# Kernel tuning notes

Hardware: AMD Instinct MI355X
Metric: run time of the kernel (lower is better)

## Reference

```python
import jax, jax.numpy as jnp
import numpy as np

EPS = 1e-5

def _ln(x):
    # non-affine LayerNorm over last dim
    m = jnp.mean(x, axis=-1, keepdims=True)
    v = jnp.var(x, axis=-1, keepdims=True)
    return (x - m) / jnp.sqrt(v + EPS)

def setup_inputs() -> dict:
    key = jax.random.key(0)
    ks = jax.random.split(key, 6)
    B, D_in, H = 16384, 512, 512
    bound_i = 1.0 / np.sqrt(D_in)
    bound_h = 1.0 / np.sqrt(H)
    x = jax.random.normal(ks[0], (B, D_in), dtype=jnp.float32)
    hx = jax.random.normal(ks[1], (B, H), dtype=jnp.float32)
    W_i2h = jax.random.uniform(ks[2], (3 * H, D_in), minval=-bound_i, maxval=bound_i, dtype=jnp.float32)
    b_i2h = jax.random.uniform(ks[3], (3 * H,), minval=-bound_i, maxval=bound_i, dtype=jnp.float32)
    W_h2h = jax.random.uniform(ks[4], (3 * H, H), minval=-bound_h, maxval=bound_h, dtype=jnp.float32)
    b_h2h = jax.random.uniform(ks[5], (3 * H,), minval=-bound_h, maxval=bound_h, dtype=jnp.float32)
    return {"x": x, "hx": hx, "W_i2h": W_i2h, "b_i2h": b_i2h, "W_h2h": W_h2h, "b_h2h": b_h2h}

def reference(x, hx, W_i2h, b_i2h, W_h2h, b_h2h):
    H = hx.shape[-1]
    xt = x @ W_i2h.T + b_i2h        # [B, 3H]
    ht = hx @ W_h2h.T + b_h2h       # [B, 3H]
    x_new = xt[:, 2 * H:]
    h_new = ht[:, 2 * H:]
    gates = jax.nn.sigmoid(_ln(xt[:, : 2 * H]) + _ln(ht[:, : 2 * H]))
    r_t = gates[:, :H]
    z_t = gates[:, H:]
    n_t = jnp.tanh(_ln(x_new) + r_t * _ln(h_new))
    h_t = z_t * hx + (1.0 - z_t) * n_t
    return h_t
```

## Files before the change

### kernel.cpp

```cpp
#include <hip/hip_runtime.h>

#define M_ROWS 16384
#define N_COLS 1536
#define K_DIM  512
#define H_DIM  512

typedef __attribute__((ext_vector_type(8))) short short8;
typedef __attribute__((ext_vector_type(16))) float f32x16;

__device__ __forceinline__ unsigned short f2bf(float f) {
  unsigned u = __float_as_uint(f);
  u += 0x7fffu + ((u >> 16) & 1u);
  return (unsigned short)(u >> 16);
}
__device__ __forceinline__ float bf2f(unsigned short h) {
  return __uint_as_float(((unsigned)h) << 16);
}

__device__ __forceinline__ void gload_lds16(const void* g, void* l) {
  __builtin_amdgcn_global_load_lds((const __attribute__((address_space(1))) void*)g,
                                   (__attribute__((address_space(3))) void*)l,
                                   16, 0, 0);
}

__global__ __launch_bounds__(256) void cvt_all(
    const float* __restrict__ x, const float* __restrict__ hx,
    const float* __restrict__ Wi, const float* __restrict__ Wh,
    unsigned short* __restrict__ xb, unsigned short* __restrict__ hxb,
    unsigned short* __restrict__ Wib, unsigned short* __restrict__ Whb) {
  int i = blockIdx.x * blockDim.x + threadIdx.x;
  const float* s; unsigned short* d; int off;
  if (i < 2097152)      { s = x;  d = xb;  off = i; }
  else if (i < 4194304) { s = hx; d = hxb; off = i - 2097152; }
  else if (i < 4390912) { s = Wi; d = Wib; off = i - 4194304; }
  else                  { s = Wh; d = Whb; off = i - 4390912; }
  float4 f = ((const float4*)s)[off];
  ushort4 u;
  u.x = f2bf(f.x); u.y = f2bf(f.y); u.z = f2bf(f.z); u.w = f2bf(f.w);
  ((ushort4*)d)[off] = u;
}

__global__ __launch_bounds__(256, 4) void gemm_bf16(
    const unsigned short* __restrict__ xb, const unsigned short* __restrict__ hxb,
    const unsigned short* __restrict__ Wib, const unsigned short* __restrict__ Whb,
    const float* __restrict__ b_i2h, const float* __restrict__ b_h2h,
    unsigned short* __restrict__ xt, unsigned short* __restrict__ ht) {
  const int mat = blockIdx.z;
  const unsigned short* A  = mat ? hxb : xb;
  const unsigned short* Bw = mat ? Whb : Wib;
  const float* bias        = mat ? b_h2h : b_i2h;
  unsigned short* outp     = mat ? ht : xt;

  const int m0 = blockIdx.x * 128;
  const int n0 = blockIdx.y * 128;

  __shared__ short lds[2 * 128 * 64];
  short* ldsA = lds;
  short* ldsB = lds + 128 * 64;

  const int t = threadIdx.x;
  const int w = t >> 6, lane = t & 63;
  const int w_row = w >> 1, w_col = w & 1;
  const int l31 = lane & 31, h = lane >> 5;

  f32x16 acc[2][2];
#pragma unroll
  for (int i = 0; i < 2; ++i)
#pragma unroll
    for (int j = 0; j < 2; ++j)
#pragma unroll
      for (int r = 0; r < 16; ++r) acc[i][j][r] = 0.f;

  const int srow = lane >> 3;
  const int scol = ((lane & 7) ^ srow) * 8;

  for (int k0 = 0; k0 < K_DIM; k0 += 64) {
#pragma unroll
    for (int q = 0; q < 4; ++q) {
      const int base_row = w * 32 + q * 8;
      gload_lds16(A  + (size_t)(m0 + base_row + srow) * K_DIM + k0 + scol,
                  &ldsA[base_row * 64]);
      gload_lds16(Bw + (size_t)(n0 + base_row + srow) * K_DIM + k0 + scol,
                  &ldsB[base_row * 64]);
    }
    __syncthreads();
#pragma unroll
    for (int kk = 0; kk < 4; ++kk) {
      const int chunk = ((kk * 2 + h) ^ (l31 & 7)) * 8;
      short8 af[2], bf[2];
#pragma unroll
      for (int i = 0; i < 2; ++i)
        af[i] = *(const short8*)&ldsA[(w_row * 64 + i * 32 + l31) * 64 + chunk];
#pragma unroll
      for (int j = 0; j < 2; ++j)
        bf[j] = *(const short8*)&ldsB[(w_col * 64 + j * 32 + l31) * 64 + chunk];
#pragma unroll
      for (int i = 0; i < 2; ++i)
#pragma unroll
        for (int j = 0; j < 2; ++j)
          acc[i][j] = __builtin_amdgcn_mfma_f32_32x32x16_bf16(af[i], bf[j], acc[i][j], 0, 0, 0);
    }
    __syncthreads();
  }

  const float biasj0 = bias[n0 + w_col * 64 + l31];
  const float biasj1 = bias[n0 + w_col * 64 + 32 + l31];

#pragma unroll
  for (int i = 0; i < 2; ++i) {
#pragma unroll
    for (int g = 0; g < 4; ++g) {
#pragma unroll
      for (int d = 0; d < 4; ++d) {
        const int reg = g * 4 + d;
        const int row = d + 8 * g + 4 * h;
        ushort2 pk;
        pk.x = f2bf(acc[i][0][reg] + biasj0);
        pk.y = f2bf(acc[i][1][reg] + biasj1);
        *(ushort2*)(outp + (size_t)(m0 + w_row * 64 + i * 32 + row) * N_COLS +
                    n0 + w_col * 64 + 2 * l31) = pk;
      }
    }
  }
}

__global__ __launch_bounds__(256, 6) void finalize_kernel(
    const unsigned short* __restrict__ xt, const unsigned short* __restrict__ ht,
    const unsigned short* __restrict__ hxb, float* __restrict__ out) {
  const int w = threadIdx.x >> 6, lane = threadIdx.x & 63;
  const int b = blockIdx.x * 4 + w;
  const size_t rb = (size_t)b * N_COLS;

  const short8 sxr = *(const short8*)&xt[rb + 8 * lane];
  const short8 sxz = *(const short8*)&xt[rb + 512 + 8 * lane];
  const short8 sxn = *(const short8*)&xt[rb + 1024 + 8 * lane];
  const short8 shr = *(const short8*)&ht[rb + 8 * lane];
  const short8 shz = *(const short8*)&ht[rb + 512 + 8 * lane];
  const short8 shn = *(const short8*)&ht[rb + 1024 + 8 * lane];
  const int base4 = 64 * (lane >> 3) + 4 * (lane & 7);
  const unsigned short* hxrow = hxb + (size_t)b * H_DIM;
  const ushort4 hx0u = *(const ushort4*)&hxrow[base4];
  const ushort4 hx1u = *(const ushort4*)&hxrow[base4 + 32];

  float pr[8] = {0.f, 0.f, 0.f, 0.f, 0.f, 0.f, 0.f, 0.f};
#pragma unroll
  for (int k = 0; k < 8; ++k) {
    const float xr = bf2f((unsigned short)sxr[k]);
    const float xz = bf2f((unsigned short)sxz[k]);
    const float xn = bf2f((unsigned short)sxn[k]);
    const float hr = bf2f((unsigned short)shr[k]);
    const float hz = bf2f((unsigned short)shz[k]);
    const float hn = bf2f((unsigned short)shn[k]);
    pr[0] += xr + xz;
    pr[1] += xr * xr + xz * xz;
    pr[2] += xn;
    pr[3] += xn * xn;
    pr[4] += hr + hz;
    pr[5] += hr * hr + hz * hz;
    pr[6] += hn;
    pr[7] += hn * hn;
  }
#pragma unroll
  for (int msk = 1; msk < 64; msk <<= 1)
#pragma unroll
    for (int k = 0; k < 8; ++k) pr[k] += __shfl_xor(pr[k], msk);

  const float inv2H = 1.f / 1024.f, invH = 1.f / 512.f;
  const float mx0 = pr[0] * inv2H;
  const float ix0 = rsqrtf(pr[1] * inv2H - mx0 * mx0 + 1e-5f);
  const float mx1 = pr[2] * invH;
  const float ix1 = rsqrtf(pr[3] * invH - mx1 * mx1 + 1e-5f);
  const float mh0 = pr[4] * inv2H;
  const float ih0 = rsqrtf(pr[5] * inv2H - mh0 * mh0 + 1e-5f);
  const float mh1 = pr[6] * invH;
  const float ih1 = rsqrtf(pr[7] * invH - mh1 * mh1 + 1e-5f);

  auto calc = [&](float xrv, float xzv, float xnv, float hrv, float hzv,
                  float hnv, float hxs) -> float {
    float ar = (xrv - mx0) * ix0 + (hrv - mh0) * ih0;
    float az = (xzv - mx0) * ix0 + (hzv - mh0) * ih0;
    float r = 1.f / (1.f + __expf(-ar));
    float z = 1.f / (1.f + __expf(-az));
    float arg = (xnv - mx1) * ix1 + r * ((hnv - mh1) * ih1);
    float e2 = __expf(2.f * arg);
    float nn = (e2 - 1.f) / (e2 + 1.f);
    return z * hxs + (1.f - z) * nn;
  };

  float* orow = out + (size_t)b * H_DIM;

  float4 r0, r1;
  float* r0p = (float*)&r0;
  float* r1p = (float*)&r1;
  const unsigned short hx0a[4] = {hx0u.x, hx0u.y, hx0u.z, hx0u.w};
  const unsigned short hx1a[4] = {hx1u.x, hx1u.y, hx1u.z, hx1u.w};
#pragma unroll
  for (int k = 0; k < 4; ++k) {
    r0p[k] = calc(bf2f((unsigned short)sxr[2 * k]), bf2f((unsigned short)sxz[2 * k]),
                  bf2f((unsigned short)sxn[2 * k]), bf2f((unsigned short)shr[2 * k]),
                  bf2f((unsigned short)shz[2 * k]), bf2f((unsigned short)shn[2 * k]),
                  bf2f(hx0a[k]));
    r1p[k] = calc(bf2f((unsigned short)sxr[2 * k + 1]), bf2f((unsigned short)sxz[2 * k + 1]),
                  bf2f((unsigned short)sxn[2 * k + 1]), bf2f((unsigned short)shr[2 * k + 1]),
                  bf2f((unsigned short)shz[2 * k + 1]), bf2f((unsigned short)shn[2 * k + 1]),
                  bf2f(hx1a[k]));
  }
  *(float4*)&orow[base4] = r0;
  *(float4*)&orow[base4 + 32] = r1;
}

extern "C" void kernel_launch(void* const* d_in, const int* in_sizes, int n_in,
                              void* d_out, int out_size, void* d_ws, size_t ws_size,
                              hipStream_t stream) {
  const float* x  = (const float*)d_in[0];
  const float* hx = (const float*)d_in[1];
  const float* Wi = (const float*)d_in[2];
  const float* bi = (const float*)d_in[3];
  const float* Wh = (const float*)d_in[4];
  const float* bh = (const float*)d_in[5];
  float* out = (float*)d_out;

  char* ws = (char*)d_ws;
  unsigned short* xb  = (unsigned short*)(ws);
  unsigned short* hxb = (unsigned short*)(ws + 16777216);
  unsigned short* Wib = (unsigned short*)(ws + 33554432);
  unsigned short* Whb = (unsigned short*)(ws + 35127296);
  unsigned short* xt  = (unsigned short*)(ws + 36700160);
  unsigned short* ht  = (unsigned short*)(ws + 87031808);

  cvt_all<<<17920, 256, 0, stream>>>(x, hx, Wi, Wh, xb, hxb, Wib, Whb);

  gemm_bf16<<<dim3(M_ROWS / 128, N_COLS / 128, 2), 256, 0, stream>>>(
      xb, hxb, Wib, Whb, bi, bh, xt, ht);

  finalize_kernel<<<M_ROWS / 4, 256, 0, stream>>>(xt, ht, hxb, out);
}
```

Before: 206.4 us.

## Fuse GRU finalize into GEMM via per-row-block atomic completion counter

Each GEMM block now computes four N-tiles for one 128-row panel and one matrix, which reuses the A panel from cache across tiles. Blocks that share a row panel increment an atomic counter, and the last of the six runs the LayerNorm/GRU finalize for those 128 rows. This removes the separate finalize launch and lets finalize overlap with other blocks' GEMM work. The cost is a grid of only 768 blocks with serial tiles, which lowers parallelism, and the finalize tail runs on a single block per panel.

New measurement: 441.8 us. +114.0%, slower.

```diff
diff --git a/kernel.cpp b/kernel.cpp
--- a/kernel.cpp
+++ b/kernel.cpp
@@ -27,8 +27,10 @@
     const float* __restrict__ x, const float* __restrict__ hx,
     const float* __restrict__ Wi, const float* __restrict__ Wh,
     unsigned short* __restrict__ xb, unsigned short* __restrict__ hxb,
-    unsigned short* __restrict__ Wib, unsigned short* __restrict__ Whb) {
+    unsigned short* __restrict__ Wib, unsigned short* __restrict__ Whb,
+    int* __restrict__ cnt) {
   int i = blockIdx.x * blockDim.x + threadIdx.x;
+  if (blockIdx.x == 0 && threadIdx.x < 128) cnt[threadIdx.x] = 0;
   const float* s; unsigned short* d; int off;
   if (i < 2097152)      { s = x;  d = xb;  off = i; }
   else if (i < 4194304) { s = hx; d = hxb; off = i - 2097152; }
@@ -40,173 +42,185 @@
   ((ushort4*)d)[off] = u;
 }
 
-__global__ __launch_bounds__(256, 4) void gemm_bf16(
+__global__ __launch_bounds__(256, 4) void gemm_fin(
     const unsigned short* __restrict__ xb, const unsigned short* __restrict__ hxb,
     const unsigned short* __restrict__ Wib, const unsigned short* __restrict__ Whb,
     const float* __restrict__ b_i2h, const float* __restrict__ b_h2h,
-    unsigned short* __restrict__ xt, unsigned short* __restrict__ ht) {
-  const int mat = blockIdx.z;
+    unsigned short* __restrict__ xt, unsigned short* __restrict__ ht,
+    float* __restrict__ out, int* __restrict__ cnt) {
+  const int bid = blockIdx.x;
+  const int mp  = bid / 6;
+  const int rem = bid % 6;
+  const int mat = rem & 1;
+  const int ng  = rem >> 1;
+  const int m0  = mp * 128;
+
   const unsigned short* A  = mat ? hxb : xb;
   const unsigned short* Bw = mat ? Whb : Wib;
   const float* bias        = mat ? b_h2h : b_i2h;
   unsigned short* outp     = mat ? ht : xt;
 
-  const int m0 = blockIdx.x * 128;
-  const int n0 = blockIdx.y * 128;
-
   __shared__ short lds[2 * 128 * 64];
   short* ldsA = lds;
   short* ldsB = lds + 128 * 64;
+  __shared__ int dofin;
 
   const int t = threadIdx.x;
   const int w = t >> 6, lane = t & 63;
   const int w_row = w >> 1, w_col = w & 1;
   const int l31 = lane & 31, h = lane >> 5;
-
-  f32x16 acc[2][2];
-#pragma unroll
-  for (int i = 0; i < 2; ++i)
-#pragma unroll
-    for (int j = 0; j < 2; ++j)
-#pragma unroll
-      for (int r = 0; r < 16; ++r) acc[i][j][r] = 0.f;
-
   const int srow = lane >> 3;
   const int scol = ((lane & 7) ^ srow) * 8;
 
-  for (int k0 = 0; k0 < K_DIM; k0 += 64) {
-#pragma unroll
-    for (int q = 0; q < 4; ++q) {
-      const int base_row = w * 32 + q * 8;
-      gload_lds16(A  + (size_t)(m0 + base_row + srow) * K_DIM + k0 + scol,
-                  &ldsA[base_row * 64]);
-      gload_lds16(Bw + (size_t)(n0 + base_row + srow) * K_DIM + k0 + scol,
-                  &ldsB[base_row * 64]);
-    }
-    __syncthreads();
-#pragma unroll
-    for (int kk = 0; kk < 4; ++kk) {
-      const int chunk = ((kk * 2 + h) ^ (l31 & 7)) * 8;
-      short8 af[2], bf[2];
-#pragma unroll
-      for (int i = 0; i < 2; ++i)
-        af[i] = *(const short8*)&ldsA[(w_row * 64 + i * 32 + l31) * 64 + chunk];
+  for (int nt = 0; nt < 4; ++nt) {
+    const int n0 = (ng * 4 + nt) * 128;
+
+    f32x16 acc[2][2];
+#pragma unroll
+    for (int i = 0; i < 2; ++i)
 #pragma unroll
       for (int j = 0; j < 2; ++j)
-        bf[j] = *(const short8*)&ldsB[(w_col * 64 + j * 32 + l31) * 64 + chunk];
-#pragma unroll
-      for (int i = 0; i < 2; ++i)
+#pragma unroll
+        for (int r = 0; r < 16; ++r) acc[i][j][r] = 0.f;
+
+    for (int k0 = 0; k0 < K_DIM; k0 += 64) {
+#pragma unroll
+      for (int q = 0; q < 4; ++q) {
+        const int base_row = w * 32 + q * 8;
+        gload_lds16(A  + (size_t)(m0 + base_row + srow) * K_DIM + k0 + scol,
+                    &ldsA[base_row * 64]);
+        gload_lds16(Bw + (size_t)(n0 + base_row + srow) * K_DIM + k0 + scol,
+                    &ldsB[base_row * 64]);
+      }
+      __syncthreads();
+#pragma unroll
+      for (int kk = 0; kk < 4; ++kk) {
+        const int chunk = ((kk * 2 + h) ^ (l31 & 7)) * 8;
+        short8 af[2], bfr[2];
+#pragma unroll
+        for (int i = 0; i < 2; ++i)
+          af[i] = *(const short8*)&ldsA[(w_row * 64 + i * 32 + l31) * 64 + chunk];
 #pragma unroll
         for (int j = 0; j < 2; ++j)
-          acc[i][j] = __builtin_amdgcn_mfma_f32_32x32x16_bf16(af[i], bf[j], acc[i][j], 0, 0, 0);
-    }
-    __syncthreads();
+          bfr[j] = *(const short8*)&ldsB[(w_col * 64 + j * 32 + l31) * 64 + chunk];
+#pragma unroll
+        for (int i = 0; i < 2; ++i)
+#pragma unroll
+          for (int j = 0; j < 2; ++j)
+            acc[i][j] = __builtin_amdgcn_mfma_f32_32x32x16_bf16(af[i], bfr[j], acc[i][j], 0, 0, 0);
+      }
+      __syncthreads();
+    }
+
+    const float biasj0 = bias[n0 + w_col * 64 + l31];
+    const float biasj1 = bias[n0 + w_col * 64 + 32 + l31];
+#pragma unroll
+    for (int i = 0; i < 2; ++i) {
+#pragma unroll
+      for (int g = 0; g < 4; ++g) {
+#pragma unroll
+        for (int d = 0; d < 4; ++d) {
+          const int reg = g * 4 + d;
+          const int row = d + 8 * g + 4 * h;
+          ushort2 pk;
+          pk.x = f2bf(acc[i][0][reg] + biasj0);
+          pk.y = f2bf(acc[i][1][reg] + biasj1);
+          *(ushort2*)(outp + (size_t)(m0 + w_row * 64 + i * 32 + row) * N_COLS +
+                      n0 + w_col * 64 + 2 * l31) = pk;
+        }
+      }
+    }
   }
 
-  const float biasj0 = bias[n0 + w_col * 64 + l31];
-  const float biasj1 = bias[n0 + w_col * 64 + 32 + l31];
-
-#pragma unroll
-  for (int i = 0; i < 2; ++i) {
-#pragma unroll
-    for (int g = 0; g < 4; ++g) {
-#pragma unroll
-      for (int d = 0; d < 4; ++d) {
-        const int reg = g * 4 + d;
-        const int row = d + 8 * g + 4 * h;
-        ushort2 pk;
-        pk.x = f2bf(acc[i][0][reg] + biasj0);
-        pk.y = f2bf(acc[i][1][reg] + biasj1);
-        *(ushort2*)(outp + (size_t)(m0 + w_row * 64 + i * 32 + row) * N_COLS +
-                    n0 + w_col * 64 + 2 * l31) = pk;
-      }
-    }
+  __syncthreads();
+  if (t == 0) {
+    __threadfence();
+    dofin = (atomicAdd(&cnt[mp], 1) == 5);
   }
-}
-
-__global__ __launch_bounds__(256, 6) void finalize_kernel(
-    const unsigned short* __restrict__ xt, const unsigned short* __restrict__ ht,
-    const unsigned short* __restrict__ hxb, float* __restrict__ out) {
-  const int w = threadIdx.x >> 6, lane = threadIdx.x & 63;
-  const int b = blockIdx.x * 4 + w;
-  const size_t rb = (size_t)b * N_COLS;
-
-  const short8 sxr = *(const short8*)&xt[rb + 8 * lane];
-  const short8 sxz = *(const short8*)&xt[rb + 512 + 8 * lane];
-  const short8 sxn = *(const short8*)&xt[rb + 1024 + 8 * lane];
-  const short8 shr = *(const short8*)&ht[rb + 8 * lane];
-  const short8 shz = *(const short8*)&ht[rb + 512 + 8 * lane];
-  const short8 shn = *(const short8*)&ht[rb + 1024 + 8 * lane];
+  __syncthreads();
+  if (!dofin) return;
+  __threadfence();
+
   const int base4 = 64 * (lane >> 3) + 4 * (lane & 7);
-  const unsigned short* hxrow = hxb + (size_t)b * H_DIM;
-  const ushort4 hx0u = *(const ushort4*)&hxrow[base4];
-  const ushort4 hx1u = *(const ushort4*)&hxrow[base4 + 32];
-
-  float pr[8] = {0.f, 0.f, 0.f, 0.f, 0.f, 0.f, 0.f, 0.f};
-#pragma unroll
-  for (int k = 0; k < 8; ++k) {
-    const float xr = bf2f((unsigned short)sxr[k]);
-    const float xz = bf2f((unsigned short)sxz[k]);
-    const float xn = bf2f((unsigned short)sxn[k]);
-    const float hr = bf2f((unsigned short)shr[k]);
-    const float hz = bf2f((unsigned short)shz[k]);
-    const float hn = bf2f((unsigned short)shn[k]);
-    pr[0] += xr + xz;
-    pr[1] += xr * xr + xz * xz;
-    pr[2] += xn;
-    pr[3] += xn * xn;
-    pr[4] += hr + hz;
-    pr[5] += hr * hr + hz * hz;
-    pr[6] += hn;
-    pr[7] += hn * hn;
+  for (int r = 0; r < 32; ++r) {
+    const int b = m0 + w * 32 + r;
+    const size_t rb = (size_t)b * N_COLS;
+
+    const short8 sxr = *(const short8*)&xt[rb + 8 * lane];
+    const short8 sxz = *(const short8*)&xt[rb + 512 + 8 * lane];
+    const short8 sxn = *(const short8*)&xt[rb + 1024 + 8 * lane];
+    const short8 shr = *(const short8*)&ht[rb + 8 * lane];
+    const short8 shz = *(const short8*)&ht[rb + 512 + 8 * lane];
+    const short8 shn = *(const short8*)&ht[rb + 1024 + 8 * lane];
+    const unsigned short* hxrow = hxb + (size_t)b * H_DIM;
+    const ushort4 hx0u = *(const ushort4*)&hxrow[base4];
+    const ushort4 hx1u = *(const ushort4*)&hxrow[base4 + 32];
+
+    float pr[8] = {0.f, 0.f, 0.f, 0.f, 0.f, 0.f, 0.f, 0.f};
+#pragma unroll
+    for (int k = 0; k < 8; ++k) {
+      const float xr = bf2f((unsigned short)sxr[k]);
+      const float xz = bf2f((unsigned short)sxz[k]);
+      const float xn = bf2f((unsigned short)sxn[k]);
+      const float hr = bf2f((unsigned short)shr[k]);
+      const float hz = bf2f((unsigned short)shz[k]);
+      const float hn = bf2f((unsigned short)shn[k]);
+      pr[0] += xr + xz;
+      pr[1] += xr * xr + xz * xz;
+      pr[2] += xn;
+      pr[3] += xn * xn;
+      pr[4] += hr + hz;
+      pr[5] += hr * hr + hz * hz;
+      pr[6] += hn;
+      pr[7] += hn * hn;
+    }
+#pragma unroll
+    for (int msk = 1; msk < 64; msk <<= 1)
+#pragma unroll
+      for (int k = 0; k < 8; ++k) pr[k] += __shfl_xor(pr[k], msk);
+
+    const float inv2H = 1.f / 1024.f, invH = 1.f / 512.f;
+    const float mx0 = pr[0] * inv2H;
+    const float ix0 = rsqrtf(pr[1] * inv2H - mx0 * mx0 + 1e-5f);
+    const float mx1 = pr[2] * invH;
+    const float ix1 = rsqrtf(pr[3] * invH - mx1 * mx1 + 1e-5f);
+    const float mh0 = pr[4] * inv2H;
+    const float ih0 = rsqrtf(pr[5] * inv2H - mh0 * mh0 + 1e-5f);
+    const float mh1 = pr[6] * invH;
+    const float ih1 = rsqrtf(pr[7] * invH - mh1 * mh1 + 1e-5f);
+
+    auto calc = [&](float xrv, float xzv, float xnv, float hrv, float hzv,
+                    float hnv, float hxs) -> float {
+      float ar = (xrv - mx0) * ix0 + (hrv - mh0) * ih0;
+      float az = (xzv - mx0) * ix0 + (hzv - mh0) * ih0;
+      float rr = 1.f / (1.f + __expf(-ar));
+      float zz = 1.f / (1.f + __expf(-az));
+      float arg = (xnv - mx1) * ix1 + rr * ((hnv - mh1) * ih1);
+      float e2 = __expf(2.f * arg);
+      float nn = (e2 - 1.f) / (e2 + 1.f);
+      return zz * hxs + (1.f - zz) * nn;
+    };
+
+    float* orow = out + (size_t)b * H_DIM;
+    float4 r0, r1;
+    float* r0p = (float*)&r0;
+    float* r1p = (float*)&r1;
+    const unsigned short hx0a[4] = {hx0u.x, hx0u.y, hx0u.z, hx0u.w};
+    const unsigned short hx1a[4] = {hx1u.x, hx1u.y, hx1u.z, hx1u.w};
+#pragma unroll
+    for (int k = 0; k < 4; ++k) {
+      r0p[k] = calc(bf2f((unsigned short)sxr[2 * k]), bf2f((unsigned short)sxz[2 * k]),
+                    bf2f((unsigned short)sxn[2 * k]), bf2f((unsigned short)shr[2 * k]),
+                    bf2f((unsigned short)shz[2 * k]), bf2f((unsigned short)shn[2 * k]),
+                    bf2f(hx0a[k]));
+      r1p[k] = calc(bf2f((unsigned short)sxr[2 * k + 1]), bf2f((unsigned short)sxz[2 * k + 1]),
+                    bf2f((unsigned short)sxn[2 * k + 1]), bf2f((unsigned short)shr[2 * k + 1]),
+                    bf2f((unsigned short)shz[2 * k + 1]), bf2f((unsigned short)shn[2 * k + 1]),
+                    bf2f(hx1a[k]));
+    }
+    *(float4*)&orow[base4] = r0;
+    *(float4*)&orow[base4 + 32] = r1;
   }
-#pragma unroll
-  for (int msk = 1; msk < 64; msk <<= 1)
-#pragma unroll
-    for (int k = 0; k < 8; ++k) pr[k] += __shfl_xor(pr[k], msk);
-
-  const float inv2H = 1.f / 1024.f, invH = 1.f / 512.f;
-  const float mx0 = pr[0] * inv2H;
-  const float ix0 = rsqrtf(pr[1] * inv2H - mx0 * mx0 + 1e-5f);
-  const float mx1 = pr[2] * invH;
-  const float ix1 = rsqrtf(pr[3] * invH - mx1 * mx1 + 1e-5f);
-  const float mh0 = pr[4] * inv2H;
-  const float ih0 = rsqrtf(pr[5] * inv2H - mh0 * mh0 + 1e-5f);
-  const float mh1 = pr[6] * invH;
-  const float ih1 = rsqrtf(pr[7] * invH - mh1 * mh1 + 1e-5f);
-
-  auto calc = [&](float xrv, float xzv, float xnv, float hrv, float hzv,
-                  float hnv, float hxs) -> float {
-    float ar = (xrv - mx0) * ix0 + (hrv - mh0) * ih0;
-    float az = (xzv - mx0) * ix0 + (hzv - mh0) * ih0;
-    float r = 1.f / (1.f + __expf(-ar));
-    float z = 1.f / (1.f + __expf(-az));
-    float arg = (xnv - mx1) * ix1 + r * ((hnv - mh1) * ih1);
-    float e2 = __expf(2.f * arg);
-    float nn = (e2 - 1.f) / (e2 + 1.f);
-    return z * hxs + (1.f - z) * nn;
-  };
-
-  float* orow = out + (size_t)b * H_DIM;
-
-  float4 r0, r1;
-  float* r0p = (float*)&r0;
-  float* r1p = (float*)&r1;
-  const unsigned short hx0a[4] = {hx0u.x, hx0u.y, hx0u.z, hx0u.w};
-  const unsigned short hx1a[4] = {hx1u.x, hx1u.y, hx1u.z, hx1u.w};
-#pragma unroll
-  for (int k = 0; k < 4; ++k) {
-    r0p[k] = calc(bf2f((unsigned short)sxr[2 * k]), bf2f((unsigned short)sxz[2 * k]),
-                  bf2f((unsigned short)sxn[2 * k]), bf2f((unsigned short)shr[2 * k]),
-                  bf2f((unsigned short)shz[2 * k]), bf2f((unsigned short)shn[2 * k]),
-                  bf2f(hx0a[k]));
-    r1p[k] = calc(bf2f((unsigned short)sxr[2 * k + 1]), bf2f((unsigned short)sxz[2 * k + 1]),
-                  bf2f((unsigned short)sxn[2 * k + 1]), bf2f((unsigned short)shr[2 * k + 1]),
-                  bf2f((unsigned short)shz[2 * k + 1]), bf2f((unsigned short)shn[2 * k + 1]),
-                  bf2f(hx1a[k]));
-  }
-  *(float4*)&orow[base4] = r0;
-  *(float4*)&orow[base4 + 32] = r1;
 }
 
 extern "C" void kernel_launch(void* const* d_in, const int* in_sizes, int n_in,
@@ -227,11 +241,9 @@
   unsigned short* Whb = (unsigned short*)(ws + 35127296);
   unsigned short* xt  = (unsigned short*)(ws + 36700160);
   unsigned short* ht  = (unsigned short*)(ws + 87031808);
-
-  cvt_all<<<17920, 256, 0, stream>>>(x, hx, Wi, Wh, xb, hxb, Wib, Whb);
-
-  gemm_bf16<<<dim3(M_ROWS / 128, N_COLS / 128, 2), 256, 0, stream>>>(
-      xb, hxb, Wib, Whb, bi, bh, xt, ht);
-
-  finalize_kernel<<<M_ROWS / 4, 256, 0, stream>>>(xt, ht, hxb, out);
-}
+  int* cnt            = (int*)(ws + 137363456);
+
+  cvt_all<<<17920, 256, 0, stream>>>(x, hx, Wi, Wh, xb, hxb, Wib, Whb, cnt);
+
+  gemm_fin<<<768, 256, 0, stream>>>(xb, hxb, Wib, Whb, bi, bh, xt, ht, out, cnt);
+}
```

## Rewrite GEMM as 256x256 tile, 8-wave double-buffered pipelined kernel

Applied to the files above, without the earlier changes.

The bf16 GEMM moves from 128x128 tiles with 4 waves to 256x256 tiles with 8 waves. K tiles are double-buffered in LDS and split into quadrant phases, so the global-to-LDS loads for later tiles overlap the MFMA work, using explicit vmcnt waits, barriers and s_setprio. Past the last K tile, each wave issues dummy loads into a scratch LDS area so the vmcnt counts stay uniform. The output column mapping changes, and the finalize kernel's hx and output indexing are updated to match it. The goals are more data reuse per tile and latency hiding, at the cost of higher register and LDS pressure and fewer blocks in the grid.

Result: no change. 208.0 us (+0.8%).

```diff
diff --git a/kernel.cpp b/kernel.cpp
--- a/kernel.cpp
+++ b/kernel.cpp
@@ -40,7 +40,7 @@
   ((ushort4*)d)[off] = u;
 }
 
-__global__ __launch_bounds__(256, 4) void gemm_bf16(
+__global__ __launch_bounds__(512, 2) void gemm_bf16(
     const unsigned short* __restrict__ xb, const unsigned short* __restrict__ hxb,
     const unsigned short* __restrict__ Wib, const unsigned short* __restrict__ Whb,
     const float* __restrict__ b_i2h, const float* __restrict__ b_h2h,
@@ -51,74 +51,164 @@
   const float* bias        = mat ? b_h2h : b_i2h;
   unsigned short* outp     = mat ? ht : xt;
 
-  const int m0 = blockIdx.x * 128;
-  const int n0 = blockIdx.y * 128;
-
-  __shared__ short lds[2 * 128 * 64];
-  short* ldsA = lds;
-  short* ldsB = lds + 128 * 64;
+  const int m0 = blockIdx.x * 256;
+  const int n0 = blockIdx.y * 256;
+
+  __shared__ short lds[69632];
 
   const int t = threadIdx.x;
   const int w = t >> 6, lane = t & 63;
-  const int w_row = w >> 1, w_col = w & 1;
+  const int wr = w >> 2;
+  const int wc = w & 3;
   const int l31 = lane & 31, h = lane >> 5;
-
-  f32x16 acc[2][2];
-#pragma unroll
-  for (int i = 0; i < 2; ++i)
-#pragma unroll
-    for (int j = 0; j < 2; ++j)
-#pragma unroll
-      for (int r = 0; r < 16; ++r) acc[i][j][r] = 0.f;
-
   const int srow = lane >> 3;
   const int scol = ((lane & 7) ^ srow) * 8;
 
-  for (int k0 = 0; k0 < K_DIM; k0 += 64) {
-#pragma unroll
-    for (int q = 0; q < 4; ++q) {
-      const int base_row = w * 32 + q * 8;
-      gload_lds16(A  + (size_t)(m0 + base_row + srow) * K_DIM + k0 + scol,
-                  &ldsA[base_row * 64]);
-      gload_lds16(Bw + (size_t)(n0 + base_row + srow) * K_DIM + k0 + scol,
-                  &ldsB[base_row * 64]);
+  auto stA = [&](int T, int hh) {
+    if (T < 8) {
+      short* dst = &lds[(T & 1) * 16384 + hh * 8192];
+      const unsigned short* sp =
+          A + (size_t)(m0 + hh * 128 + w * 8 + srow) * K_DIM + T * 64 + scol;
+      gload_lds16(sp, &dst[(w * 8) * 64]);
+      gload_lds16(sp + (size_t)64 * K_DIM, &dst[(64 + w * 8) * 64]);
+    } else {
+      gload_lds16(A + (size_t)srow * K_DIM + scol, &lds[65536 + w * 512]);
+      gload_lds16(A + (size_t)srow * K_DIM + scol, &lds[65536 + w * 512]);
     }
-    __syncthreads();
-#pragma unroll
-    for (int kk = 0; kk < 4; ++kk) {
-      const int chunk = ((kk * 2 + h) ^ (l31 & 7)) * 8;
-      short8 af[2], bf[2];
-#pragma unroll
-      for (int i = 0; i < 2; ++i)
-        af[i] = *(const short8*)&ldsA[(w_row * 64 + i * 32 + l31) * 64 + chunk];
-#pragma unroll
-      for (int j = 0; j < 2; ++j)
-        bf[j] = *(const short8*)&ldsB[(w_col * 64 + j * 32 + l31) * 64 + chunk];
-#pragma unroll
-      for (int i = 0; i < 2; ++i)
-#pragma unroll
-        for (int j = 0; j < 2; ++j)
-          acc[i][j] = __builtin_amdgcn_mfma_f32_32x32x16_bf16(af[i], bf[j], acc[i][j], 0, 0, 0);
+  };
+  auto stB = [&](int T, int hh) {
+    if (T < 8) {
+      short* dst = &lds[32768 + (T & 1) * 16384 + hh * 8192];
+      const unsigned short* sp =
+          Bw + (size_t)(n0 + hh * 128 + w * 8 + srow) * K_DIM + T * 64 + scol;
+      gload_lds16(sp, &dst[(w * 8) * 64]);
+      gload_lds16(sp + (size_t)64 * K_DIM, &dst[(64 + w * 8) * 64]);
+    } else {
+      gload_lds16(Bw + (size_t)srow * K_DIM + scol, &lds[65536 + w * 512]);
+      gload_lds16(Bw + (size_t)srow * K_DIM + scol, &lds[65536 + w * 512]);
     }
-    __syncthreads();
+  };
+
+  f32x16 acc[2][2][2];
+#pragma unroll
+  for (int a = 0; a < 2; ++a)
+#pragma unroll
+    for (int b = 0; b < 2; ++b)
+#pragma unroll
+      for (int c = 0; c < 2; ++c)
+#pragma unroll
+        for (int r = 0; r < 16; ++r) acc[a][b][c][r] = 0.f;
+
+  stA(0, 0); stB(0, 0); stB(0, 1); stA(0, 1); stA(1, 0); stB(1, 0);
+  asm volatile("s_waitcnt vmcnt(8)" ::: "memory");
+  __builtin_amdgcn_s_barrier();
+  asm volatile("" ::: "memory");
+
+  int ch[4];
+#pragma unroll
+  for (int kk = 0; kk < 4; ++kk) ch[kk] = ((kk * 2 + h) ^ (l31 & 7)) * 8;
+
+#pragma unroll 1
+  for (int kt = 0; kt < 8; ++kt) {
+    const short* lA = &lds[(kt & 1) * 16384];
+    const short* lB = &lds[32768 + (kt & 1) * 16384];
+    short8 af[2][4], bf0[4], bf1[4];
+
+#pragma unroll
+    for (int i2 = 0; i2 < 2; ++i2)
+#pragma unroll
+      for (int kk = 0; kk < 4; ++kk)
+        af[i2][kk] = *(const short8*)&lA[(wr * 64 + i2 * 32 + l31) * 64 + ch[kk]];
+#pragma unroll
+    for (int kk = 0; kk < 4; ++kk)
+      bf0[kk] = *(const short8*)&lB[(wc * 32 + l31) * 64 + ch[kk]];
+    stB(kt + 1, 1);
+    asm volatile("s_waitcnt vmcnt(8)" ::: "memory");
+    __builtin_amdgcn_s_barrier();
+    asm volatile("" ::: "memory");
+    __builtin_amdgcn_s_setprio(1);
+#pragma unroll
+    for (int i2 = 0; i2 < 2; ++i2)
+#pragma unroll
+      for (int kk = 0; kk < 4; ++kk)
+        acc[0][0][i2] = __builtin_amdgcn_mfma_f32_32x32x16_bf16(af[i2][kk], bf0[kk], acc[0][0][i2], 0, 0, 0);
+    __builtin_amdgcn_s_setprio(0);
+    asm volatile("" ::: "memory");
+    __builtin_amdgcn_s_barrier();
+    asm volatile("" ::: "memory");
+
+#pragma unroll
+    for (int kk = 0; kk < 4; ++kk)
+      bf1[kk] = *(const short8*)&lB[(128 + wc * 32 + l31) * 64 + ch[kk]];
+    stA(kt + 1, 1);
+    asm volatile("s_waitcnt vmcnt(8)" ::: "memory");
+    __builtin_amdgcn_s_barrier();
+    asm volatile("" ::: "memory");
+    __builtin_amdgcn_s_setprio(1);
+#pragma unroll
+    for (int i2 = 0; i2 < 2; ++i2)
+#pragma unroll
+      for (int kk = 0; kk < 4; ++kk)
+        acc[0][1][i2] = __builtin_amdgcn_mfma_f32_32x32x16_bf16(af[i2][kk], bf1[kk], acc[0][1][i2], 0, 0, 0);
+    __builtin_amdgcn_s_setprio(0);
+    asm volatile("" ::: "memory");
+    __builtin_amdgcn_s_barrier();
+    asm volatile("" ::: "memory");
+
+#pragma unroll
+    for (int i2 = 0; i2 < 2; ++i2)
+#pragma unroll
+      for (int kk = 0; kk < 4; ++kk)
+        af[i2][kk] = *(const short8*)&lA[(128 + wr * 64 + i2 * 32 + l31) * 64 + ch[kk]];
+    stA(kt + 2, 0);
+    asm volatile("s_waitcnt vmcnt(8)" ::: "memory");
+    __builtin_amdgcn_s_barrier();
+    asm volatile("" ::: "memory");
+    __builtin_amdgcn_s_setprio(1);
+#pragma unroll
+    for (int i2 = 0; i2 < 2; ++i2)
+#pragma unroll
+      for (int kk = 0; kk < 4; ++kk)
+        acc[1][0][i2] = __builtin_amdgcn_mfma_f32_32x32x16_bf16(af[i2][kk], bf0[kk], acc[1][0][i2], 0, 0, 0);
+    __builtin_amdgcn_s_setprio(0);
+    asm volatile("" ::: "memory");
+    __builtin_amdgcn_s_barrier();
+    asm volatile("" ::: "memory");
+
+    stB(kt + 2, 0);
+    asm volatile("s_waitcnt vmcnt(8)" ::: "memory");
+    __builtin_amdgcn_s_barrier();
+    asm volatile("" ::: "memory");
+    __builtin_amdgcn_s_setprio(1);
+#pragma unroll
+    for (int i2 = 0; i2 < 2; ++i2)
+#pragma unroll
+      for (int kk = 0; kk < 4; ++kk)
+        acc[1][1][i2] = __builtin_amdgcn_mfma_f32_32x32x16_bf16(af[i2][kk], bf1[kk], acc[1][1][i2], 0, 0, 0);
+    __builtin_amdgcn_s_setprio(0);
+    asm volatile("" ::: "memory");
+    __builtin_amdgcn_s_barrier();
+    asm volatile("" ::: "memory");
   }
 
-  const float biasj0 = bias[n0 + w_col * 64 + l31];
-  const float biasj1 = bias[n0 + w_col * 64 + 32 + l31];
-
-#pragma unroll
-  for (int i = 0; i < 2; ++i) {
-#pragma unroll
-    for (int g = 0; g < 4; ++g) {
-#pragma unroll
-      for (int d = 0; d < 4; ++d) {
-        const int reg = g * 4 + d;
-        const int row = d + 8 * g + 4 * h;
-        ushort2 pk;
-        pk.x = f2bf(acc[i][0][reg] + biasj0);
-        pk.y = f2bf(acc[i][1][reg] + biasj1);
-        *(ushort2*)(outp + (size_t)(m0 + w_row * 64 + i * 32 + row) * N_COLS +
-                    n0 + w_col * 64 + 2 * l31) = pk;
+  const int cQ = wc * 32 + l31;
+  const float bias0 = bias[n0 + cQ];
+  const float bias1 = bias[n0 + 128 + cQ];
+#pragma unroll
+  for (int Qm = 0; Qm < 2; ++Qm) {
+#pragma unroll
+    for (int i2 = 0; i2 < 2; ++i2) {
+#pragma unroll
+      for (int g = 0; g < 4; ++g) {
+#pragma unroll
+        for (int d = 0; d < 4; ++d) {
+          const int reg = g * 4 + d;
+          const int row = m0 + Qm * 128 + wr * 64 + i2 * 32 + (d + 8 * g + 4 * h);
+          ushort2 pk;
+          pk.x = f2bf(acc[Qm][0][i2][reg] + bias0);
+          pk.y = f2bf(acc[Qm][1][i2][reg] + bias1);
+          *(ushort2*)(outp + (size_t)row * N_COLS + n0 + 2 * cQ) = pk;
+        }
       }
     }
   }
@@ -137,10 +227,10 @@
   const short8 shr = *(const short8*)&ht[rb + 8 * lane];
   const short8 shz = *(const short8*)&ht[rb + 512 + 8 * lane];
   const short8 shn = *(const short8*)&ht[rb + 1024 + 8 * lane];
-  const int base4 = 64 * (lane >> 3) + 4 * (lane & 7);
+  const int base8 = 256 * (lane >> 5) + 4 * (lane & 31);
   const unsigned short* hxrow = hxb + (size_t)b * H_DIM;
-  const ushort4 hx0u = *(const ushort4*)&hxrow[base4];
-  const ushort4 hx1u = *(const ushort4*)&hxrow[base4 + 32];
+  const ushort4 hx0u = *(const ushort4*)&hxrow[base8];
+  const ushort4 hx1u = *(const ushort4*)&hxrow[base8 + 128];
 
   float pr[8] = {0.f, 0.f, 0.f, 0.f, 0.f, 0.f, 0.f, 0.f};
 #pragma unroll
@@ -188,7 +278,6 @@
   };
 
   float* orow = out + (size_t)b * H_DIM;
-
   float4 r0, r1;
   float* r0p = (float*)&r0;
   float* r1p = (float*)&r1;
@@ -205,8 +294,8 @@
                   bf2f((unsigned short)shz[2 * k + 1]), bf2f((unsigned short)shn[2 * k + 1]),
                   bf2f(hx1a[k]));
   }
-  *(float4*)&orow[base4] = r0;
-  *(float4*)&orow[base4 + 32] = r1;
+  *(float4*)&orow[base8] = r0;
+  *(float4*)&orow[base8 + 128] = r1;
 }
 
 extern "C" void kernel_launch(void* const* d_in, const int* in_sizes, int n_in,
@@ -230,7 +319,7 @@
 
   cvt_all<<<17920, 256, 0, stream>>>(x, hx, Wi, Wh, xb, hxb, Wib, Whb);
 
-  gemm_bf16<<<dim3(M_ROWS / 128, N_COLS / 128, 2), 256, 0, stream>>>(
+  gemm_bf16<<<dim3(M_ROWS / 256, N_COLS / 256, 2), 512, 0, stream>>>(
       xb, hxb, Wib, Whb, bi, bh, xt, ht);
 
   finalize_kernel<<<M_ROWS / 4, 256, 0, stream>>>(xt, ht, hxb, out);
```

## Fuse activation conversion, both GEMMs and GRU finalize into one kernel

Applied to the files above, without the earlier changes.

Replaces the separate activation-conversion, GEMM and finalize kernels with one persistent-style kernel. Each 512-thread block owns 64 rows: it converts the fp32 x/hx rows to bf16 directly into LDS, runs both GEMMs across all 1536 output columns, then reads its just-written xt/ht rows back for the LayerNorm/gating epilogue. Only the weights are still converted in a separate pass. The aim is to drop the bf16 activation round trip and to read xt/ht while they are likely still cache-resident. In exchange there is one block per CU, no overlap between weight loads and MFMA, and every block re-streams the full weight matrices.

Result: slower. 219.5 us (+6.4%).

```diff
diff --git a/kernel.cpp b/kernel.cpp
--- a/kernel.cpp
+++ b/kernel.cpp
@@ -16,6 +16,11 @@
 __device__ __forceinline__ float bf2f(unsigned short h) {
   return __uint_as_float(((unsigned)h) << 16);
 }
+__device__ __forceinline__ unsigned cvt_pk_bf16(float lo, float hi) {
+  unsigned r;
+  asm("v_cvt_pk_bf16_f32 %0, %1, %2" : "=v"(r) : "v"(lo), "v"(hi));
+  return r;
+}
 
 __device__ __forceinline__ void gload_lds16(const void* g, void* l) {
   __builtin_amdgcn_global_load_lds((const __attribute__((address_space(1))) void*)g,
@@ -23,190 +28,203 @@
                                    16, 0, 0);
 }
 
-__global__ __launch_bounds__(256) void cvt_all(
-    const float* __restrict__ x, const float* __restrict__ hx,
+__global__ __launch_bounds__(256) void cvt_w(
     const float* __restrict__ Wi, const float* __restrict__ Wh,
-    unsigned short* __restrict__ xb, unsigned short* __restrict__ hxb,
     unsigned short* __restrict__ Wib, unsigned short* __restrict__ Whb) {
   int i = blockIdx.x * blockDim.x + threadIdx.x;
   const float* s; unsigned short* d; int off;
-  if (i < 2097152)      { s = x;  d = xb;  off = i; }
-  else if (i < 4194304) { s = hx; d = hxb; off = i - 2097152; }
-  else if (i < 4390912) { s = Wi; d = Wib; off = i - 4194304; }
-  else                  { s = Wh; d = Whb; off = i - 4390912; }
+  if (i < 196608) { s = Wi; d = Wib; off = i; }
+  else            { s = Wh; d = Whb; off = i - 196608; }
   float4 f = ((const float4*)s)[off];
   ushort4 u;
   u.x = f2bf(f.x); u.y = f2bf(f.y); u.z = f2bf(f.z); u.w = f2bf(f.w);
   ((ushort4*)d)[off] = u;
 }
 
-__global__ __launch_bounds__(256, 4) void gemm_bf16(
-    const unsigned short* __restrict__ xb, const unsigned short* __restrict__ hxb,
+__global__ __launch_bounds__(512, 1) void fused(
+    const float* __restrict__ x, const float* __restrict__ hx,
     const unsigned short* __restrict__ Wib, const unsigned short* __restrict__ Whb,
     const float* __restrict__ b_i2h, const float* __restrict__ b_h2h,
-    unsigned short* __restrict__ xt, unsigned short* __restrict__ ht) {
-  const int mat = blockIdx.z;
-  const unsigned short* A  = mat ? hxb : xb;
-  const unsigned short* Bw = mat ? Whb : Wib;
-  const float* bias        = mat ? b_h2h : b_i2h;
-  unsigned short* outp     = mat ? ht : xt;
-
-  const int m0 = blockIdx.x * 128;
-  const int n0 = blockIdx.y * 128;
-
-  __shared__ short lds[2 * 128 * 64];
-  short* ldsA = lds;
-  short* ldsB = lds + 128 * 64;
+    unsigned short* __restrict__ xt, unsigned short* __restrict__ ht,
+    float* __restrict__ out) {
+  const int m0 = blockIdx.x * 64;
+
+  __shared__ short ldsA[8][64][64];
+  __shared__ short ldsB[512 * 64];
 
   const int t = threadIdx.x;
   const int w = t >> 6, lane = t & 63;
-  const int w_row = w >> 1, w_col = w & 1;
   const int l31 = lane & 31, h = lane >> 5;
-
-  f32x16 acc[2][2];
-#pragma unroll
-  for (int i = 0; i < 2; ++i)
-#pragma unroll
-    for (int j = 0; j < 2; ++j)
-#pragma unroll
-      for (int r = 0; r < 16; ++r) acc[i][j][r] = 0.f;
-
   const int srow = lane >> 3;
   const int scol = ((lane & 7) ^ srow) * 8;
 
-  for (int k0 = 0; k0 < K_DIM; k0 += 64) {
-#pragma unroll
-    for (int q = 0; q < 4; ++q) {
-      const int base_row = w * 32 + q * 8;
-      gload_lds16(A  + (size_t)(m0 + base_row + srow) * K_DIM + k0 + scol,
-                  &ldsA[base_row * 64]);
-      gload_lds16(Bw + (size_t)(n0 + base_row + srow) * K_DIM + k0 + scol,
-                  &ldsB[base_row * 64]);
-    }
+  for (int mat = 0; mat < 2; ++mat) {
+    const float* A32         = mat ? hx : x;
+    const unsigned short* Bw = mat ? Whb : Wib;
+    const float* bias        = mat ? b_h2h : b_i2h;
+    unsigned short* outp     = mat ? ht : xt;
+
     __syncthreads();
-#pragma unroll
-    for (int kk = 0; kk < 4; ++kk) {
-      const int chunk = ((kk * 2 + h) ^ (l31 & 7)) * 8;
-      short8 af[2], bf[2];
+    {
+      const int arow = t >> 3, ac = t & 7;
+      const int pc = (ac ^ (arow & 7)) * 8;
+#pragma unroll
+      for (int kt = 0; kt < 8; ++kt) {
+        const float* src = A32 + (size_t)(m0 + arow) * K_DIM + kt * 64 + ac * 8;
+        float4 f0 = *(const float4*)src;
+        float4 f1 = *(const float4*)(src + 4);
+        uint4 u;
+        u.x = cvt_pk_bf16(f0.x, f0.y);
+        u.y = cvt_pk_bf16(f0.z, f0.w);
+        u.z = cvt_pk_bf16(f1.x, f1.y);
+        u.w = cvt_pk_bf16(f1.z, f1.w);
+        *(uint4*)&ldsA[kt][arow][pc] = u;
+      }
+    }
+
+    for (int p = 0; p < 3; ++p) {
+      const int n0 = p * 512;
+      f32x16 acc[2][2];
 #pragma unroll
       for (int i = 0; i < 2; ++i)
-        af[i] = *(const short8*)&ldsA[(w_row * 64 + i * 32 + l31) * 64 + chunk];
-#pragma unroll
-      for (int j = 0; j < 2; ++j)
-        bf[j] = *(const short8*)&ldsB[(w_col * 64 + j * 32 + l31) * 64 + chunk];
-#pragma unroll
-      for (int i = 0; i < 2; ++i)
 #pragma unroll
         for (int j = 0; j < 2; ++j)
-          acc[i][j] = __builtin_amdgcn_mfma_f32_32x32x16_bf16(af[i], bf[j], acc[i][j], 0, 0, 0);
-    }
-    __syncthreads();
+#pragma unroll
+          for (int r = 0; r < 16; ++r) acc[i][j][r] = 0.f;
+
+      for (int kt = 0; kt < 8; ++kt) {
+        __syncthreads();
+#pragma unroll
+        for (int q = 0; q < 8; ++q) {
+          const int br = w * 64 + q * 8;
+          gload_lds16(Bw + (size_t)(n0 + br + srow) * K_DIM + kt * 64 + scol,
+                      &ldsB[br * 64]);
+        }
+        __syncthreads();
+#pragma unroll
+        for (int kk = 0; kk < 4; ++kk) {
+          const int chunk = ((kk * 2 + h) ^ (l31 & 7)) * 8;
+          short8 af[2], bfr[2];
+#pragma unroll
+          for (int i = 0; i < 2; ++i)
+            af[i] = *(const short8*)&ldsA[kt][i * 32 + l31][chunk];
+#pragma unroll
+          for (int j = 0; j < 2; ++j)
+            bfr[j] = *(const short8*)&ldsB[(w * 64 + j * 32 + l31) * 64 + chunk];
+#pragma unroll
+          for (int i = 0; i < 2; ++i)
+#pragma unroll
+            for (int j = 0; j < 2; ++j)
+              acc[i][j] = __builtin_amdgcn_mfma_f32_32x32x16_bf16(af[i], bfr[j], acc[i][j], 0, 0, 0);
+        }
+      }
+
+      const float biasj0 = bias[n0 + w * 64 + l31];
+      const float biasj1 = bias[n0 + w * 64 + 32 + l31];
+#pragma unroll
+      for (int i = 0; i < 2; ++i) {
+#pragma unroll
+        for (int g = 0; g < 4; ++g) {
+#pragma unroll
+          for (int d = 0; d < 4; ++d) {
+            const int reg = g * 4 + d;
+            const int row = d + 8 * g + 4 * h;
+            ushort2 pk;
+            pk.x = f2bf(acc[i][0][reg] + biasj0);
+            pk.y = f2bf(acc[i][1][reg] + biasj1);
+            *(ushort2*)(outp + (size_t)(m0 + i * 32 + row) * N_COLS +
+                        n0 + w * 64 + 2 * l31) = pk;
+          }
+        }
+      }
+      __syncthreads();
+    }
   }
 
-  const float biasj0 = bias[n0 + w_col * 64 + l31];
-  const float biasj1 = bias[n0 + w_col * 64 + 32 + l31];
-
-#pragma unroll
-  for (int i = 0; i < 2; ++i) {
-#pragma unroll
-    for (int g = 0; g < 4; ++g) {
-#pragma unroll
-      for (int d = 0; d < 4; ++d) {
-        const int reg = g * 4 + d;
-        const int row = d + 8 * g + 4 * h;
-        ushort2 pk;
-        pk.x = f2bf(acc[i][0][reg] + biasj0);
-        pk.y = f2bf(acc[i][1][reg] + biasj1);
-        *(ushort2*)(outp + (size_t)(m0 + w_row * 64 + i * 32 + row) * N_COLS +
-                    n0 + w_col * 64 + 2 * l31) = pk;
-      }
-    }
+  __threadfence_block();
+  __syncthreads();
+
+  const int base4 = 64 * (lane >> 3) + 4 * (lane & 7);
+#pragma unroll 1
+  for (int rr = 0; rr < 8; ++rr) {
+    const int b = m0 + w * 8 + rr;
+    const size_t rb = (size_t)b * N_COLS;
+
+    const short8 sxr = *(const short8*)&xt[rb + 8 * lane];
+    const short8 sxz = *(const short8*)&xt[rb + 512 + 8 * lane];
+    const short8 sxn = *(const short8*)&xt[rb + 1024 + 8 * lane];
+    const short8 shr = *(const short8*)&ht[rb + 8 * lane];
+    const short8 shz = *(const short8*)&ht[rb + 512 + 8 * lane];
+    const short8 shn = *(const short8*)&ht[rb + 1024 + 8 * lane];
+    const float* hxrow = hx + (size_t)b * H_DIM;
+    const float4 hx0 = *(const float4*)&hxrow[base4];
+    const float4 hx1 = *(const float4*)&hxrow[base4 + 32];
+
+    float pr[8] = {0.f, 0.f, 0.f, 0.f, 0.f, 0.f, 0.f, 0.f};
+#pragma unroll
+    for (int k = 0; k < 8; ++k) {
+      const float xr = bf2f((unsigned short)sxr[k]);
+      const float xz = bf2f((unsigned short)sxz[k]);
+      const float xn = bf2f((unsigned short)sxn[k]);
+      const float hr = bf2f((unsigned short)shr[k]);
+      const float hz = bf2f((unsigned short)shz[k]);
+      const float hn = bf2f((unsigned short)shn[k]);
+      pr[0] += xr + xz;
+      pr[1] += xr * xr + xz * xz;
+      pr[2] += xn;
+      pr[3] += xn * xn;
+      pr[4] += hr + hz;
+      pr[5] += hr * hr + hz * hz;
+      pr[6] += hn;
+      pr[7] += hn * hn;
+    }
+#pragma unroll
+    for (int msk = 1; msk < 64; msk <<= 1)
+#pragma unroll
+      for (int k = 0; k < 8; ++k) pr[k] += __shfl_xor(pr[k], msk);
+
+    const float inv2H = 1.f / 1024.f, invH = 1.f / 512.f;
+    const float mx0 = pr[0] * inv2H;
+    const float ix0 = rsqrtf(pr[1] * inv2H - mx0 * mx0 + 1e-5f);
+    const float mx1 = pr[2] * invH;
+    const float ix1 = rsqrtf(pr[3] * invH - mx1 * mx1 + 1e-5f);
+    const float mh0 = pr[4] * inv2H;
+    const float ih0 = rsqrtf(pr[5] * inv2H - mh0 * mh0 + 1e-5f);
+    const float mh1 = pr[6] * invH;
+    const float ih1 = rsqrtf(pr[7] * invH - mh1 * mh1 + 1e-5f);
+
+    auto calc = [&](float xrv, float xzv, float xnv, float hrv, float hzv,
+                    float hnv, float hxs) -> float {
+      float ar = (xrv - mx0) * ix0 + (hrv - mh0) * ih0;
+      float az = (xzv - mx0) * ix0 + (hzv - mh0) * ih0;
+      float r = 1.f / (1.f + __expf(-ar));
+      float z = 1.f / (1.f + __expf(-az));
+      float arg = (xnv - mx1) * ix1 + r * ((hnv - mh1) * ih1);
+      float e2 = __expf(2.f * arg);
+      float nn = (e2 - 1.f) / (e2 + 1.f);
+      return z * hxs + (1.f - z) * nn;
+    };
+
+    float* orow = out + (size_t)b * H_DIM;
+    float4 r0, r1;
+    float* r0p = (float*)&r0;
+    float* r1p = (float*)&r1;
+    const float* h0p = (const float*)&hx0;
+    const float* h1p = (const float*)&hx1;
+#pragma unroll
+    for (int k = 0; k < 4; ++k) {
+      r0p[k] = calc(bf2f((unsigned short)sxr[2 * k]), bf2f((unsigned short)sxz[2 * k]),
+                    bf2f((unsigned short)sxn[2 * k]), bf2f((unsigned short)shr[2 * k]),
+                    bf2f((unsigned short)shz[2 * k]), bf2f((unsigned short)shn[2 * k]),
+                    h0p[k]);
+      r1p[k] = calc(bf2f((unsigned short)sxr[2 * k + 1]), bf2f((unsigned short)sxz[2 * k + 1]),
+                    bf2f((unsigned short)sxn[2 * k + 1]), bf2f((unsigned short)shr[2 * k + 1]),
+                    bf2f((unsigned short)shz[2 * k + 1]), bf2f((unsigned short)shn[2 * k + 1]),
+                    h1p[k]);
+    }
+    *(float4*)&orow[base4] = r0;
+    *(float4*)&orow[base4 + 32] = r1;
   }
-}
-
-__global__ __launch_bounds__(256, 6) void finalize_kernel(
-    const unsigned short* __restrict__ xt, const unsigned short* __restrict__ ht,
-    const unsigned short* __restrict__ hxb, float* __restrict__ out) {
-  const int w = threadIdx.x >> 6, lane = threadIdx.x & 63;
-  const int b = blockIdx.x * 4 + w;
-  const size_t rb = (size_t)b * N_COLS;
-
-  const short8 sxr = *(const short8*)&xt[rb + 8 * lane];
-  const short8 sxz = *(const short8*)&xt[rb + 512 + 8 * lane];
-  const short8 sxn = *(const short8*)&xt[rb + 1024 + 8 * lane];
-  const short8 shr = *(const short8*)&ht[rb + 8 * lane];
-  const short8 shz = *(const short8*)&ht[rb + 512 + 8 * lane];
-  const short8 shn = *(const short8*)&ht[rb + 1024 + 8 * lane];
-  const int base4 = 64 * (lane >> 3) + 4 * (lane & 7);
-  const unsigned short* hxrow = hxb + (size_t)b * H_DIM;
-  const ushort4 hx0u = *(const ushort4*)&hxrow[base4];
-  const ushort4 hx1u = *(const ushort4*)&hxrow[base4 + 32];
-
-  float pr[8] = {0.f, 0.f, 0.f, 0.f, 0.f, 0.f, 0.f, 0.f};
-#pragma unroll
-  for (int k = 0; k < 8; ++k) {
-    const float xr = bf2f((unsigned short)sxr[k]);
-    const float xz = bf2f((unsigned short)sxz[k]);
-    const float xn = bf2f((unsigned short)sxn[k]);
-    const float hr = bf2f((unsigned short)shr[k]);
-    const float hz = bf2f((unsigned short)shz[k]);
-    const float hn = bf2f((unsigned short)shn[k]);
-    pr[0] += xr + xz;
-    pr[1] += xr * xr + xz * xz;
-    pr[2] += xn;
-    pr[3] += xn * xn;
-    pr[4] += hr + hz;
-    pr[5] += hr * hr + hz * hz;
-    pr[6] += hn;
-    pr[7] += hn * hn;
-  }
-#pragma unroll
-  for (int msk = 1; msk < 64; msk <<= 1)
-#pragma unroll
-    for (int k = 0; k < 8; ++k) pr[k] += __shfl_xor(pr[k], msk);
-
-  const float inv2H = 1.f / 1024.f, invH = 1.f / 512.f;
-  const float mx0 = pr[0] * inv2H;
-  const float ix0 = rsqrtf(pr[1] * inv2H - mx0 * mx0 + 1e-5f);
-  const float mx1 = pr[2] * invH;
-  const float ix1 = rsqrtf(pr[3] * invH - mx1 * mx1 + 1e-5f);
-  const float mh0 = pr[4] * inv2H;
-  const float ih0 = rsqrtf(pr[5] * inv2H - mh0 * mh0 + 1e-5f);
-  const float mh1 = pr[6] * invH;
-  const float ih1 = rsqrtf(pr[7] * invH - mh1 * mh1 + 1e-5f);
-
-  auto calc = [&](float xrv, float xzv, float xnv, float hrv, float hzv,
-                  float hnv, float hxs) -> float {
-    float ar = (xrv - mx0) * ix0 + (hrv - mh0) * ih0;
-    float az = (xzv - mx0) * ix0 + (hzv - mh0) * ih0;
-    float r = 1.f / (1.f + __expf(-ar));
-    float z = 1.f / (1.f + __expf(-az));
-    float arg = (xnv - mx1) * ix1 + r * ((hnv - mh1) * ih1);
-    float e2 = __expf(2.f * arg);
-    float nn = (e2 - 1.f) / (e2 + 1.f);
-    return z * hxs + (1.f - z) * nn;
-  };
-
-  float* orow = out + (size_t)b * H_DIM;
-
-  float4 r0, r1;
-  float* r0p = (float*)&r0;
-  float* r1p = (float*)&r1;
-  const unsigned short hx0a[4] = {hx0u.x, hx0u.y, hx0u.z, hx0u.w};
-  const unsigned short hx1a[4] = {hx1u.x, hx1u.y, hx1u.z, hx1u.w};
-#pragma unroll
-  for (int k = 0; k < 4; ++k) {
-    r0p[k] = calc(bf2f((unsigned short)sxr[2 * k]), bf2f((unsigned short)sxz[2 * k]),
-                  bf2f((unsigned short)sxn[2 * k]), bf2f((unsigned short)shr[2 * k]),
-                  bf2f((unsigned short)shz[2 * k]), bf2f((unsigned short)shn[2 * k]),
-                  bf2f(hx0a[k]));
-    r1p[k] = calc(bf2f((unsigned short)sxr[2 * k + 1]), bf2f((unsigned short)sxz[2 * k + 1]),
-                  bf2f((unsigned short)sxn[2 * k + 1]), bf2f((unsigned short)shr[2 * k + 1]),
-                  bf2f((unsigned short)shz[2 * k + 1]), bf2f((unsigned short)shn[2 * k + 1]),
-                  bf2f(hx1a[k]));
-  }
-  *(float4*)&orow[base4] = r0;
-  *(float4*)&orow[base4 + 32] = r1;
 }
 
 extern "C" void kernel_launch(void* const* d_in, const int* in_sizes, int n_in,
@@ -221,17 +239,12 @@
   float* out = (float*)d_out;
 
   char* ws = (char*)d_ws;
-  unsigned short* xb  = (unsigned short*)(ws);
-  unsigned short* hxb = (unsigned short*)(ws + 16777216);
-  unsigned short* Wib = (unsigned short*)(ws + 33554432);
-  unsigned short* Whb = (unsigned short*)(ws + 35127296);
-  unsigned short* xt  = (unsigned short*)(ws + 36700160);
-  unsigned short* ht  = (unsigned short*)(ws + 87031808);
-
-  cvt_all<<<17920, 256, 0, stream>>>(x, hx, Wi, Wh, xb, hxb, Wib, Whb);
-
-  gemm_bf16<<<dim3(M_ROWS / 128, N_COLS / 128, 2), 256, 0, stream>>>(
-      xb, hxb, Wib, Whb, bi, bh, xt, ht);
-
-  finalize_kernel<<<M_ROWS / 4, 256, 0, stream>>>(xt, ht, hxb, out);
-}
+  unsigned short* Wib = (unsigned short*)(ws);
+  unsigned short* Whb = (unsigned short*)(ws + 1572864);
+  unsigned short* xt  = (unsigned short*)(ws + 3145728);
+  unsigned short* ht  = (unsigned short*)(ws + 53477376);
+
+  cvt_w<<<1536, 256, 0, stream>>>(Wi, Wh, Wib, Whb);
+
+  fused<<<256, 512, 0, stream>>>(x, hx, Wib, Whb, bi, bh, xt, ht, out);
+}
```
